# Performance work log

Measured on AMD Instinct MI355X. Metric: run time of the kernel, lower is better.

## Reference

```python
import jax, jax.numpy as jnp
import numpy as np
from jax import lax

B, C, H, W = 32, 128, 56, 56
SIZE = C * H * W
EPS = 1e-5
SLOPE = 0.1


def setup_inputs() -> dict:
    key = jax.random.key(0)
    ks = jax.random.split(key, 12)
    return {
        "ax": jax.random.normal(ks[0], (B, C, H, W), dtype=jnp.float32),
        "mx": jax.random.normal(ks[1], (B, C, H, W), dtype=jnp.float32),
        # grouped conv1d (groups=SIZE, k=2, no bias) == per-position pair weights [SIZE, 2]
        "cfc_w": jax.random.normal(ks[2], (SIZE, 2), dtype=jnp.float32) * 0.1,
        # BatchNorm1d (eval mode) params over SIZE channels
        "bn_gamma": jax.random.normal(ks[3], (SIZE,), dtype=jnp.float32) * 0.1 + 1.0,
        "bn_beta": jax.random.normal(ks[4], (SIZE,), dtype=jnp.float32) * 0.1,
        "bn_mean": jax.random.normal(ks[5], (SIZE,), dtype=jnp.float32) * 0.1,
        "bn_var": jax.random.uniform(ks[6], (SIZE,), dtype=jnp.float32, minval=0.5, maxval=1.5),
        # conv3x3, C->C, bias
        "conv_w": jax.random.normal(ks[7], (C, C, 3, 3), dtype=jnp.float32) * (1.0 / np.sqrt(C * 9)),
        "conv_b": jax.random.normal(ks[8], (C,), dtype=jnp.float32) * 0.01,
        # BatchNorm2d (eval mode) params over C channels
        "bn2_gamma": jax.random.normal(ks[9], (C,), dtype=jnp.float32) * 0.1 + 1.0,
        "bn2_beta": jax.random.normal(ks[10], (C,), dtype=jnp.float32) * 0.1,
        "bn2_mean": jax.random.normal(ks[11], (C,), dtype=jnp.float32) * 0.1,
        "bn2_var": jax.random.uniform(jax.random.fold_in(key, 99), (C,), dtype=jnp.float32, minval=0.5, maxval=1.5),
    }


def reference(ax, mx, cfc_w, bn_gamma, bn_beta, bn_mean, bn_var,
              conv_w, conv_b, bn2_gamma, bn2_beta, bn2_mean, bn2_var):
    b, c, h, w = ax.shape
    a = ax.reshape(b, -1)  # [B, SIZE]
    m = mx.reshape(b, -1)
    # degenerate grouped Conv1d(k=2, groups=SIZE): z_i = w_i0 * a_i + w_i1 * m_i
    z = cfc_w[:, 0] * a + cfc_w[:, 1] * m
    # BatchNorm1d (eval) + LeakyReLU(0.1)
    z = (z - bn_mean) * (bn_gamma / jnp.sqrt(bn_var + EPS)) + bn_beta
    z = jax.nn.leaky_relu(z, SLOPE).reshape(b, c, h, w)
    # conv3x3 (stride 1, pad 1) + bias
    y = lax.conv_general_dilated(z, conv_w, window_strides=(1, 1),
                                 padding=((1, 1), (1, 1)),
                                 dimension_numbers=("NCHW", "OIHW", "NCHW"))
    y = y + conv_b[None, :, None, None]
    # BatchNorm2d (eval) + LeakyReLU(0.1)
    scale = (bn2_gamma / jnp.sqrt(bn2_var + EPS))[None, :, None, None]
    y = (y - bn2_mean[None, :, None, None]) * scale + bn2_beta[None, :, None, None]
    return jax.nn.leaky_relu(y, SLOPE)
```

## Files before the change

kernel.cpp:

```cpp
#include <hip/hip_runtime.h>

#define B_ 32
#define C_ 128
#define H_ 56
#define W_ 56
#define HW_ (H_*W_)
#define SIZE_ (C_*HW_)
#define NPIX_ (B_*HW_)
#define HP_ 58
#define WP_ 58
#define PLSZ_ (B_*HP_*WP_*32)
#define K_ 1152
#define EPS_ 1e-5f
#define SLOPE_ 0.1f

typedef __bf16 bf16x8 __attribute__((ext_vector_type(8)));
typedef float  f32x4  __attribute__((ext_vector_type(4)));

__device__ __forceinline__ ushort f2bf(float x) {
    union { float f; unsigned u; } v; v.f = x;
    return (ushort)((v.u + 0x7FFFu + ((v.u >> 16) & 1u)) >> 16);
}
__device__ __forceinline__ float lrelu(float z) { return z > 0.f ? z : SLOPE_ * z; }

__device__ __forceinline__ void glds16(const ushort* g, ushort* l) {
    __builtin_amdgcn_global_load_lds(
        (const __attribute__((address_space(1))) unsigned int*)g,
        (__attribute__((address_space(3))) unsigned int*)l, 16, 0, 0);
}

__global__ __launch_bounds__(256) void prep_kernel(
    const float* __restrict__ conv_w, const float* __restrict__ conv_b,
    const float* __restrict__ g2, const float* __restrict__ b2,
    const float* __restrict__ m2, const float* __restrict__ v2,
    const float2* __restrict__ cfc, const float* __restrict__ g1,
    const float* __restrict__ b1, const float* __restrict__ mu1,
    const float* __restrict__ v1,
    ushort* __restrict__ wA, float* __restrict__ scale2, float* __restrict__ shift2,
    float* __restrict__ p0, float* __restrict__ p1, float* __restrict__ p2)
{
    int tid = blockIdx.x * 256 + threadIdx.x;
    if (tid < C_ * K_) {
        int co = tid / K_;
        int k  = tid - co * K_;
        int khkw = k >> 7, ci = k & 127;
        int kh = khkw / 3, kw = khkw - 3 * kh;
        wA[((k >> 6) * C_ + co) * 64 + (k & 63)] =
            f2bf(conv_w[((co * C_ + ci) * 3 + kh) * 3 + kw]);
    }
    if (tid < C_) {
        float sc = g2[tid] * rsqrtf(v2[tid] + EPS_);
        scale2[tid] = sc;
        shift2[tid] = (conv_b[tid] - m2[tid]) * sc + b2[tid];
    }
    if (tid < SIZE_) {
        float sc = g1[tid] * rsqrtf(v1[tid] + EPS_);
        float2 wv = cfc[tid];
        p0[tid] = wv.x * sc;
        p1[tid] = wv.y * sc;
        p2[tid] = b1[tid] - mu1[tid] * sc;
    }
}

__global__ __launch_bounds__(256, 4) void zfuse_kernel(
    const float4* __restrict__ ax, const float4* __restrict__ mx,
    const float4* __restrict__ p0, const float4* __restrict__ p1,
    const float4* __restrict__ p2, ushort* __restrict__ zp)
{
    __shared__ float4 axS[4][448];
    __shared__ float4 mxS[4][448];
    __shared__ ushort tile[W_ * 132];

    const int tid = threadIdx.x;
    const int wg  = blockIdx.x;
    const int swz = (wg & 7) * 232 + (wg >> 3);
    const int hp  = swz >> 5;
    const int b   = swz & 31;
    const int rb  = (b * HP_ + hp) * (WP_ * 32);

    if (hp == 0 || hp == HP_ - 1) {
        for (int ks = 0; ks < 4; ++ks) {
            uint2* r2 = (uint2*)(zp + ks * PLSZ_ + rb);
            for (int i = tid; i < WP_ * 32 / 4; i += 256) r2[i] = make_uint2(0u, 0u);
        }
        return;
    }
    const int h  = hp - 1;
    const int wv = tid >> 6, l = tid & 63;
    const int base4 = b * (SIZE_ / 4);
    const int hb4   = h * (W_ / 4);

    #pragma unroll
    for (int j = 0; j < 7; ++j) {
        int i  = j * 64 + l;
        int cl = i / 14, w4 = i - cl * 14;
        int s4 = (wv * 32 + cl) * (HW_ / 4) + hb4 + w4;
        glds16((const ushort*)(ax + base4 + s4), (ushort*)&axS[wv][j * 64]);
        glds16((const ushort*)(mx + base4 + s4), (ushort*)&mxS[wv][j * 64]);
    }
    asm volatile("s_waitcnt vmcnt(0)" ::: "memory");
    __builtin_amdgcn_sched_barrier(0);

    #pragma unroll
    for (int u = 0; u < 7; ++u) {
        int i  = u * 64 + l;
        int cl = i / 14, w4 = i - cl * 14;
        int c  = wv * 32 + cl;
        int s4 = c * (HW_ / 4) + hb4 + w4;
        float4 a  = axS[wv][i];
        float4 m  = mxS[wv][i];
        float4 q0 = p0[s4], q1 = p1[s4], q2 = p2[s4];
        int wb = w4 * 4;
        tile[(wb + 0) * 132 + c] = f2bf(lrelu(a.x * q0.x + m.x * q1.x + q2.x));
        tile[(wb + 1) * 132 + c] = f2bf(lrelu(a.y * q0.y + m.y * q1.y + q2.y));
        tile[(wb + 2) * 132 + c] = f2bf(lrelu(a.z * q0.z + m.z * q1.z + q2.z));
        tile[(wb + 3) * 132 + c] = f2bf(lrelu(a.w * q0.w + m.w * q1.w + q2.w));
    }
    __syncthreads();

    {
        int side = (tid >> 7) & 1, ks = (tid >> 5) & 3, cc = tid & 31;
        zp[ks * PLSZ_ + rb + (side ? (WP_ - 1) * 32 : 0) + cc] = 0;
    }
    for (int j = tid; j < 1792; j += 256) {
        int ks = j / 448, r = j - ks * 448;
        int w = r >> 3, cc = r & 7;
        *(uint2*)(zp + ks * PLSZ_ + rb + (w + 1) * 32 + cc * 4) =
            *(const uint2*)(tile + w * 132 + ks * 32 + cc * 4);
    }
}

__global__ __launch_bounds__(512, 2) void conv_kernel(
    const ushort* __restrict__ zp, const ushort* __restrict__ wA,
    const float* __restrict__ scale2, const float* __restrict__ shift2,
    float* __restrict__ out)
{
    __shared__ ushort As[3][128 * 64];
    __shared__ ushort Bs[3][256 * 64];

    const int tid  = threadIdx.x;
    const int wave = tid >> 6, lane = tid & 63;
    const int l16  = lane & 15, quad = lane >> 4;
    const int bid  = blockIdx.x;
    const int pbase = ((bid & 7) * 49 + (bid >> 3)) * 256;

    const int c_swz = (lane & 7) ^ ((lane >> 3) & 7);
    const ushort* agA = wA + (16 * wave + (lane >> 3)) * 64 + c_swz * 8;

    const ushort* bgB[4];
    #pragma unroll
    for (int j = 0; j < 4; ++j) {
        int pxl = 32 * wave + 8 * j + (lane >> 3);
        int pf  = pbase + pxl;
        int bb  = pf / HW_, pi = pf - bb * HW_;
        int h   = pi / W_, w = pi - h * W_;
        bgB[j] = zp + (c_swz >> 2) * PLSZ_
                    + ((bb * HP_ + h) * WP_ + w) * 32 + (c_swz & 3) * 8;
    }

    const int cob = (wave & 1) * 64;
    const int pxb = (wave >> 1) * 64;
    const int ch0 = ((quad ^ (l16 & 7))) * 8;
    const int ch1 = ch0 ^ 32;

    f32x4 acc[4][4] = {};

#define BDEL(t) (((t) & 1) * 2 * PLSZ_ + \
                 (((((t) >> 1) / 3) * WP_ + (((t) >> 1) % 3)) * 32))

#define STAGE(t, buf) do {                                              \
        glds16(agA + (t) * 8192,        &As[buf][wave * 1024]);         \
        glds16(agA + (t) * 8192 + 512,  &As[buf][wave * 1024 + 512]);   \
        glds16(bgB[0] + BDEL(t), &Bs[buf][wave * 2048]);                \
        glds16(bgB[1] + BDEL(t), &Bs[buf][wave * 2048 + 512]);          \
        glds16(bgB[2] + BDEL(t), &Bs[buf][wave * 2048 + 1024]);         \
        glds16(bgB[3] + BDEL(t), &Bs[buf][wave * 2048 + 1536]);         \
    } while (0)

    STAGE(0, 0);
    STAGE(1, 1);

    #pragma unroll
    for (int t = 0; t < 18; ++t) {
        __builtin_amdgcn_sched_barrier(0);
        if (t < 17) asm volatile("s_waitcnt vmcnt(6)" ::: "memory");
        else        asm volatile("s_waitcnt vmcnt(0)" ::: "memory");
        __builtin_amdgcn_s_barrier();
        __builtin_amdgcn_sched_barrier(0);
        if (t <= 15) STAGE(t + 2, (t + 2) % 3);

        const int buf = t % 3;
        bf16x8 af0[4], af1[4], bf0[4], bf1[4];
        #pragma unroll
        for (int mt = 0; mt < 4; ++mt) {
            const ushort* ar = &As[buf][(cob + mt * 16 + l16) * 64];
            af0[mt] = *(const bf16x8*)(ar + ch0);
            af1[mt] = *(const bf16x8*)(ar + ch1);
        }
        #pragma unroll
        for (int nt = 0; nt < 4; ++nt) {
            const ushort* br = &Bs[buf][(pxb + nt * 16 + l16) * 64];
            bf0[nt] = *(const bf16x8*)(br + ch0);
            bf1[nt] = *(const bf16x8*)(br + ch1);
        }
        __builtin_amdgcn_s_setprio(1);
        #pragma unroll
        for (int mt = 0; mt < 4; ++mt)
            #pragma unroll
            for (int nt = 0; nt < 4; ++nt) {
                acc[mt][nt] = __builtin_amdgcn_mfma_f32_16x16x32_bf16(
                    af0[mt], bf0[nt], acc[mt][nt], 0, 0, 0);
                acc[mt][nt] = __builtin_amdgcn_mfma_f32_16x16x32_bf16(
                    af1[mt], bf1[nt], acc[mt][nt], 0, 0, 0);
            }
        __builtin_amdgcn_s_setprio(0);
    }
#undef STAGE
#undef BDEL

    int pob[4];
    #pragma unroll
    for (int nt = 0; nt < 4; ++nt) {
        int pf = pbase + pxb + nt * 16 + l16;
        int bb = pf / HW_;
        pob[nt] = bb * SIZE_ + (pf - bb * HW_);
    }
    #pragma unroll
    for (int mt = 0; mt < 4; ++mt) {
        #pragma unroll
        for (int r = 0; r < 4; ++r) {
            int co = cob + mt * 16 + quad * 4 + r;
            float sc = scale2[co], sh = shift2[co];
            #pragma unroll
            for (int nt = 0; nt < 4; ++nt) {
                float v = acc[mt][nt][r] * sc + sh;
                out[(size_t)pob[nt] + co * HW_] = lrelu(v);
            }
        }
    }
}

extern "C" void kernel_launch(void* const* d_in, const int* in_sizes, int n_in,
                              void* d_out, int out_size, void* d_ws, size_t ws_size,
                              hipStream_t stream) {
    const float* ax     = (const float*)d_in[0];
    const float* mx     = (const float*)d_in[1];
    const float* cfc    = (const float*)d_in[2];
    const float* bn_g   = (const float*)d_in[3];
    const float* bn_b   = (const float*)d_in[4];
    const float* bn_m   = (const float*)d_in[5];
    const float* bn_v   = (const float*)d_in[6];
    const float* conv_w = (const float*)d_in[7];
    const float* conv_b = (const float*)d_in[8];
    const float* g2     = (const float*)d_in[9];
    const float* b2     = (const float*)d_in[10];
    const float* m2     = (const float*)d_in[11];
    const float* v2     = (const float*)d_in[12];
    float* out = (float*)d_out;

    char* ws = (char*)d_ws;
    ushort* zp     = (ushort*)ws;
    ushort* wA     = (ushort*)(ws + 27557888);
    float*  scale2 = (float*)(ws + 27852800);
    float*  shift2 = (float*)(ws + 27853312);
    float*  p0     = (float*)(ws + 27853824);
    float*  p1     = (float*)(ws + 29459456);
    float*  p2     = (float*)(ws + 31065088);

    prep_kernel<<<dim3((SIZE_ + 255) / 256), 256, 0, stream>>>(
        conv_w, conv_b, g2, b2, m2, v2, (const float2*)cfc,
        bn_g, bn_b, bn_m, bn_v, wA, scale2, shift2, p0, p1, p2);
    zfuse_kernel<<<dim3(HP_ * B_), 256, 0, stream>>>(
        (const float4*)ax, (const float4*)mx,
        (const float4*)p0, (const float4*)p1, (const float4*)p2, zp);
    conv_kernel<<<dim3(NPIX_ / 256), 512, 0, stream>>>(zp, wA, scale2, shift2, out);
}
```

Baseline: 224.5 us.

## Replace LDS-staged conv GEMM with single-wave blocks loading fragments directly

```diff
diff --git a/kernel.cpp b/kernel.cpp
--- a/kernel.cpp
+++ b/kernel.cpp
@@ -43,10 +43,10 @@
     if (tid < C_ * K_) {
         int co = tid / K_;
         int k  = tid - co * K_;
+        int t  = k >> 5, kk = k & 31;
         int khkw = k >> 7, ci = k & 127;
         int kh = khkw / 3, kw = khkw - 3 * kh;
-        wA[((k >> 6) * C_ + co) * 64 + (k & 63)] =
-            f2bf(conv_w[((co * C_ + ci) * 3 + kh) * 3 + kw]);
+        wA[(t * C_ + co) * 32 + kk] = f2bf(conv_w[((co * C_ + ci) * 3 + kh) * 3 + kw]);
     }
     if (tid < C_) {
         float sc = g2[tid] * rsqrtf(v2[tid] + EPS_);
@@ -130,98 +130,55 @@
     }
 }
 
-__global__ __launch_bounds__(512, 2) void conv_kernel(
+__global__ __launch_bounds__(64, 4) void conv_kernel(
     const ushort* __restrict__ zp, const ushort* __restrict__ wA,
     const float* __restrict__ scale2, const float* __restrict__ shift2,
     float* __restrict__ out)
 {
-    __shared__ ushort As[3][128 * 64];
-    __shared__ ushort Bs[3][256 * 64];
-
-    const int tid  = threadIdx.x;
-    const int wave = tid >> 6, lane = tid & 63;
+    const int lane = threadIdx.x & 63;
     const int l16  = lane & 15, quad = lane >> 4;
     const int bid  = blockIdx.x;
-    const int pbase = ((bid & 7) * 49 + (bid >> 3)) * 256;
-
-    const int c_swz = (lane & 7) ^ ((lane >> 3) & 7);
-    const ushort* agA = wA + (16 * wave + (lane >> 3)) * 64 + c_swz * 8;
-
-    const ushort* bgB[4];
-    #pragma unroll
-    for (int j = 0; j < 4; ++j) {
-        int pxl = 32 * wave + 8 * j + (lane >> 3);
-        int pf  = pbase + pxl;
-        int bb  = pf / HW_, pi = pf - bb * HW_;
-        int h   = pi / W_, w = pi - h * W_;
-        bgB[j] = zp + (c_swz >> 2) * PLSZ_
-                    + ((bb * HP_ + h) * WP_ + w) * 32 + (c_swz & 3) * 8;
-    }
-
-    const int cob = (wave & 1) * 64;
-    const int pxb = (wave >> 1) * 64;
-    const int ch0 = ((quad ^ (l16 & 7))) * 8;
-    const int ch1 = ch0 ^ 32;
+    const int swz  = (bid & 7) * 392 + (bid >> 3);
+    const int pbase = (swz >> 1) * 64;
+    const int cob   = (swz & 1) * 64;
+
+    const ushort* aptr = wA + (cob + l16) * 32 + quad * 8;
+
+    const ushort* bptr[4];
+    #pragma unroll
+    for (int nt = 0; nt < 4; ++nt) {
+        int pf = pbase + nt * 16 + l16;
+        int bb = pf / HW_, pi = pf - bb * HW_;
+        int h  = pi / W_, w = pi - h * W_;
+        bptr[nt] = zp + ((bb * HP_ + h) * WP_ + w) * 32 + quad * 8;
+    }
+
+#define BOFF(t) (((t) & 3) * PLSZ_ + (((((t) >> 2) / 3) * WP_ + (((t) >> 2) % 3)) * 32))
 
     f32x4 acc[4][4] = {};
 
-#define BDEL(t) (((t) & 1) * 2 * PLSZ_ + \
-                 (((((t) >> 1) / 3) * WP_ + (((t) >> 1) % 3)) * 32))
-
-#define STAGE(t, buf) do {                                              \
-        glds16(agA + (t) * 8192,        &As[buf][wave * 1024]);         \
-        glds16(agA + (t) * 8192 + 512,  &As[buf][wave * 1024 + 512]);   \
-        glds16(bgB[0] + BDEL(t), &Bs[buf][wave * 2048]);                \
-        glds16(bgB[1] + BDEL(t), &Bs[buf][wave * 2048 + 512]);          \
-        glds16(bgB[2] + BDEL(t), &Bs[buf][wave * 2048 + 1024]);         \
-        glds16(bgB[3] + BDEL(t), &Bs[buf][wave * 2048 + 1536]);         \
-    } while (0)
-
-    STAGE(0, 0);
-    STAGE(1, 1);
-
-    #pragma unroll
-    for (int t = 0; t < 18; ++t) {
-        __builtin_amdgcn_sched_barrier(0);
-        if (t < 17) asm volatile("s_waitcnt vmcnt(6)" ::: "memory");
-        else        asm volatile("s_waitcnt vmcnt(0)" ::: "memory");
-        __builtin_amdgcn_s_barrier();
-        __builtin_amdgcn_sched_barrier(0);
-        if (t <= 15) STAGE(t + 2, (t + 2) % 3);
-
-        const int buf = t % 3;
-        bf16x8 af0[4], af1[4], bf0[4], bf1[4];
-        #pragma unroll
-        for (int mt = 0; mt < 4; ++mt) {
-            const ushort* ar = &As[buf][(cob + mt * 16 + l16) * 64];
-            af0[mt] = *(const bf16x8*)(ar + ch0);
-            af1[mt] = *(const bf16x8*)(ar + ch1);
-        }
-        #pragma unroll
-        for (int nt = 0; nt < 4; ++nt) {
-            const ushort* br = &Bs[buf][(pxb + nt * 16 + l16) * 64];
-            bf0[nt] = *(const bf16x8*)(br + ch0);
-            bf1[nt] = *(const bf16x8*)(br + ch1);
-        }
-        __builtin_amdgcn_s_setprio(1);
+    #pragma unroll
+    for (int t = 0; t < 36; ++t) {
+        bf16x8 af[4], bfr[4];
+        #pragma unroll
+        for (int mt = 0; mt < 4; ++mt)
+            af[mt] = *(const bf16x8*)(aptr + t * 4096 + mt * 512);
+        #pragma unroll
+        for (int nt = 0; nt < 4; ++nt)
+            bfr[nt] = *(const bf16x8*)(bptr[nt] + BOFF(t));
         #pragma unroll
         for (int mt = 0; mt < 4; ++mt)
             #pragma unroll
-            for (int nt = 0; nt < 4; ++nt) {
+            for (int nt = 0; nt < 4; ++nt)
                 acc[mt][nt] = __builtin_amdgcn_mfma_f32_16x16x32_bf16(
-                    af0[mt], bf0[nt], acc[mt][nt], 0, 0, 0);
-                acc[mt][nt] = __builtin_amdgcn_mfma_f32_16x16x32_bf16(
-                    af1[mt], bf1[nt], acc[mt][nt], 0, 0, 0);
-            }
-        __builtin_amdgcn_s_setprio(0);
-    }
-#undef STAGE
-#undef BDEL
+                    af[mt], bfr[nt], acc[mt][nt], 0, 0, 0);
+    }
+#undef BOFF
 
     int pob[4];
     #pragma unroll
     for (int nt = 0; nt < 4; ++nt) {
-        int pf = pbase + pxb + nt * 16 + l16;
+        int pf = pbase + nt * 16 + l16;
         int bb = pf / HW_;
         pob[nt] = bb * SIZE_ + (pf - bb * HW_);
     }
@@ -273,5 +230,5 @@
     zfuse_kernel<<<dim3(HP_ * B_), 256, 0, stream>>>(
         (const float4*)ax, (const float4*)mx,
         (const float4*)p0, (const float4*)p1, (const float4*)p2, zp);
-    conv_kernel<<<dim3(NPIX_ / 256), 512, 0, stream>>>(zp, wA, scale2, shift2, out);
-}
+    conv_kernel<<<dim3(NPIX_ / 64 * 2), 64, 0, stream>>>(zp, wA, scale2, shift2, out);
+}
```

New measurement: 267.7 us. +19.3%, slower.
